# Kernel optimization log

Measured on AMD Instinct MI355X. Metric: run time of the kernel, lower is better.

Reference implementation:

```python
import jax, jax.numpy as jnp
import numpy as np

NUM_TAGS = 5

def setup_inputs() -> dict:
    key = jax.random.key(0)
    ks = jax.random.split(key, 8)
    B, N, K, Q = 2, 5, 5, 4
    Ls, Lq, D = 128, 128, 768
    inp = {
        'support_token_embedding': jax.random.normal(ks[0], (B * N * K, Ls, D), jnp.float32),
        'query_token_embedding': jax.random.normal(ks[1], (B * N * Q, Lq, D), jnp.float32),
        'support_mask': jnp.ones((B * N * K, Ls), jnp.float32),
        'query_mask': jnp.ones((B * N * Q, Lq), jnp.float32),
        'support_entity_label': jax.random.normal(ks[2], (B * N * K, Ls, NUM_TAGS), jnp.float32),
        'proj_w': jax.random.normal(ks[3], (D, 4 * D), jnp.float32) * 0.02,
        'proj_b': jnp.zeros((D,), jnp.float32),
        'rel_w1': jax.random.normal(ks[4], (D, 4 * D), jnp.float32) * 0.02,
        'rel_b1': jnp.zeros((D,), jnp.float32),
        'rel_w2': jax.random.normal(ks[5], (1, D), jnp.float32) * 0.02,
        'rel_b2': jnp.zeros((1,), jnp.float32),
        'B': B, 'N': N, 'K': K, 'Q': Q,
    }
    return inp

def _fuse(m1, m2):
    return jnp.concatenate([m1, m2, jnp.abs(m1 - m2), m1 * m2], axis=-1)

def reference(support_token_embedding, query_token_embedding, support_mask, query_mask,
              support_entity_label, proj_w, proj_b, rel_w1, rel_b1, rel_w2, rel_b2,
              B, N, K, Q):
    D = support_token_embedding.shape[-1]
    Lq = query_token_embedding.shape[1]

    # ---- cal_bio: per-(sample,shot) tag prototypes, vectorized ----
    labels = jnp.argmax(support_entity_label, axis=-1)                 # [BNK, Ls]
    onehot = jax.nn.one_hot(labels, NUM_TAGS, dtype=jnp.float32)       # [BNK, Ls, T]
    # tag 0 ('O') is additionally gated by the support mask
    masks = jnp.concatenate([onehot[:, :, :1] * support_mask[:, :, None], onehot[:, :, 1:]], axis=2)
    sums = jnp.einsum('blt,bld->btd', masks, support_token_embedding)  # [BNK, T, D]
    cnt = jnp.sum(masks, axis=1)[:, :, None]                           # [BNK, T, 1]
    proto = jnp.where(cnt > 0, sums / jnp.maximum(cnt, 1.0), 0.0)      # [BNK, T, D]
    proto = proto.reshape(B * N, K, NUM_TAGS, D).mean(axis=1)          # mean over K shots
    proto = proto.reshape(B, N, NUM_TAGS, D)                           # support_BIO

    # ---- expand to all (query, class) pairs: batch = B*N*Q*N ----
    BQ = B * N * Q * N
    support = jnp.broadcast_to(proto[:, None], (B, N * Q, N, NUM_TAGS, D)).reshape(BQ, NUM_TAGS, D)
    query = jnp.broadcast_to(query_token_embedding.reshape(B, N * Q, 1, Lq, D),
                             (B, N * Q, N, Lq, D)).reshape(BQ, Lq, D)
    qmask = jnp.broadcast_to(query_mask.reshape(B, N * Q, 1, Lq),
                             (B, N * Q, N, Lq)).reshape(BQ, Lq, 1)
    smask = jnp.ones((BQ, NUM_TAGS, 1), jnp.float32)

    # ---- CoAttention with additive mask bias + post-softmax mask multiply ----
    att = jnp.einsum('bsd,bqd->bsq', support, query) + smask * jnp.swapaxes(qmask, 1, 2) * 100.0
    support_ = jnp.einsum('bsq,bqd->bsd', jax.nn.softmax(att, axis=2), query) * smask
    query_ = jnp.einsum('bqs,bsd->bqd', jax.nn.softmax(jnp.swapaxes(att, 1, 2), axis=2), support) * qmask

    # ---- fuse + proj + relu ----
    es = jax.nn.relu(_fuse(support, support_) @ proj_w.T + proj_b)     # [BQ, T, D]
    eq = jax.nn.relu(_fuse(query, query_) @ proj_w.T + proj_b)        # [BQ, Lq, D]

    # ---- local aggregation: masked max + mean pooling ----
    eq_agg = jnp.concatenate([jnp.max(eq, axis=1), jnp.sum(eq, axis=1) / jnp.sum(qmask, axis=1)], axis=1)
    es_agg = jnp.concatenate([jnp.max(es, axis=1), jnp.sum(es, axis=1) / jnp.sum(smask, axis=1)], axis=1)

    # ---- relation MLP ----
    cat_seq = jnp.concatenate([eq_agg, es_agg], axis=1)                # [BQ, 4D]
    h = jax.nn.relu(cat_seq @ rel_w1.T + rel_b1)
    logits = h @ rel_w2.T + rel_b2                                     # [BQ, 1]
    return logits.reshape(B * N * Q, N)
```

## Files before the change

### kernel.cpp

```cpp
#include <hip/hip_runtime.h>

typedef unsigned short u16;
typedef __attribute__((ext_vector_type(8))) short short8;
typedef __attribute__((ext_vector_type(4))) float f32x4;

#define B_   2
#define N_   5
#define K_   5
#define Q_   4
#define T_   5
#define D_   768
#define L_   128
#define BN_  (B_*N_)
#define BNK_ (B_*N_*K_)
#define BQ_  (B_*N_*Q_*N_)
#define K4_  (4*D_)
#define KFQ  1536
#define AROWS 144

#define QEMB_N  (40*128*768)
#define PROJW_N (768*3072)
#define R_PROTO1 5120
#define R_SUP    5248
#define R_PROTO2 6248
#define R_TOTAL  6400

__device__ __forceinline__ float bf2f(u16 u) {
    return __uint_as_float(((unsigned)u) << 16);
}
__device__ __forceinline__ u16 f2bf(float f) {
    unsigned u = __float_as_uint(f);
    return (u16)((u + 0x7fffu + ((u >> 16) & 1u)) >> 16);
}
__device__ __forceinline__ void gl_lds16(const u16* g, u16* l) {
    __builtin_amdgcn_global_load_lds(
        (const __attribute__((address_space(1))) unsigned int*)g,
        (__attribute__((address_space(3))) unsigned int*)l, 16, 0, 0);
}

__global__ void k_convert3(const float* __restrict__ q, const float* __restrict__ pw,
                           const float* __restrict__ rw, u16* __restrict__ qo,
                           u16* __restrict__ po, u16* __restrict__ ro) {
    const long n1 = QEMB_N / 4, n2 = PROJW_N / 4;
    const long total = n1 + 2 * n2;
    for (long i = (long)blockIdx.x * 256 + threadIdx.x; i < total; i += (long)gridDim.x * 256) {
        const float* src; u16* dst; long k;
        if (i < n1)            { src = q;  dst = qo; k = i; }
        else if (i < n1 + n2)  { src = pw; dst = po; k = i - n1; }
        else                   { src = rw; dst = ro; k = i - n1 - n2; }
        float4 v = ((const float4*)src)[k];
        u16 o[4] = {f2bf(v.x), f2bf(v.y), f2bf(v.z), f2bf(v.w)};
        *(uint2*)(dst + k * 4) = *(const uint2*)o;
    }
}

__global__ void k_proto_shot(const float* __restrict__ label, const float* __restrict__ smask,
                             const float* __restrict__ semb, float* __restrict__ proto_shot) {
    int bnk = blockIdx.x;
    int s = blockIdx.y;
    __shared__ int   s_tag[L_];
    __shared__ float s_w[L_];
    __shared__ float s_cnt[T_];
    int tid = threadIdx.x;
    if (tid < L_) {
        const float* lp = label + ((long)bnk * L_ + tid) * T_;
        float best = lp[0]; int bi = 0;
        #pragma unroll
        for (int t = 1; t < T_; ++t) { float v = lp[t]; if (v > best) { best = v; bi = t; } }
        s_tag[tid] = bi;
        s_w[tid]   = (bi == 0) ? smask[(long)bnk * L_ + tid] : 1.0f;
    }
    __syncthreads();
    if (tid < T_) {
        float c = 0.f;
        for (int l = 0; l < L_; ++l) if (s_tag[l] == tid) c += s_w[l];
        s_cnt[tid] = c;
    }
    __syncthreads();
    float acc[T_] = {};
    for (int l = 0; l < L_; ++l) {
        float w = s_w[l]; int tg = s_tag[l];
        float e = semb[((long)bnk * L_ + l) * D_ + tid + s * 256] * w;
        #pragma unroll
        for (int t = 0; t < T_; ++t) acc[t] += (tg == t) ? e : 0.0f;
    }
    int d = tid + s * 256;
    #pragma unroll
    for (int t = 0; t < T_; ++t) {
        float c = s_cnt[t];
        float v = (c > 0.f) ? acc[t] / fmaxf(c, 1.f) : 0.f;
        proto_shot[(bnk * T_ + t) * D_ + d] = v;
    }
}

__global__ void k_proto_mean(const float* __restrict__ proto_shot,
                             float* __restrict__ proto_f32, u16* __restrict__ A_all) {
    int bx = blockIdx.x;
    if (bx < 150) {
        int idx = bx * 256 + threadIdx.x;
        if (idx >= BN_ * T_ * D_) return;
        int r = idx / D_, d = idx - r * D_;
        int bn = r / T_;
        int rem = idx - bn * (T_ * D_);
        float s = 0.f;
        #pragma unroll
        for (int k = 0; k < K_; ++k) s += proto_shot[(bn * K_ + k) * (T_ * D_) + rem];
        s *= (1.f / K_);
        proto_f32[idx] = s;
        u16 b = f2bf(s);
        A_all[(size_t)(R_PROTO1 + r) * D_ + d] = b;
        A_all[(size_t)(R_PROTO2 + r) * D_ + d] = b;
    } else {
        int zidx = (bx - 150) * 256 + threadIdx.x;
        if (zidx >= 59904 + 78336) return;
        size_t off;
        if (zidx < 59904) off = (size_t)5170 * D_ + zidx;
        else              off = (size_t)6298 * D_ + (zidx - 59904);
        A_all[off] = 0;
    }
}

__global__ void k_attn(const float* __restrict__ qemb, const float* __restrict__ qmask_g,
                       const float* __restrict__ proto_f32,
                       u16* __restrict__ qf, u16* __restrict__ supA,
                       float* __restrict__ p2m_ws, float* __restrict__ qssum_ws) {
    int x = blockIdx.x;
    int xcd = x & 7, slot = x >> 3;
    int g = (slot / 5) * 8 + xcd;
    int n2 = slot % 5;
    int bq = g * 5 + n2;
    int q_idx = g;
    int bn = (bq / (N_ * Q_ * N_)) * N_ + (bq % N_);
    __shared__ float s_proto[T_ * D_];
    __shared__ float s_att[T_][L_];
    __shared__ float s_ps[T_][L_];
    __shared__ float s_p2[L_][8];
    __shared__ float s_qm[L_];
    int tid = threadIdx.x;
    int w = tid >> 6, lane = tid & 63;
    for (int i = tid; i < T_ * D_; i += 256) s_proto[i] = proto_f32[bn * T_ * D_ + i];
    if (tid < L_) s_qm[tid] = qmask_g[(long)q_idx * L_ + tid];
    __syncthreads();
    for (int p = tid; p < T_ * L_; p += 256) {
        int t = p >> 7, q = p & (L_ - 1);
        const float* pp = s_proto + t * D_;
        const float4* qp = (const float4*)(qemb + ((size_t)q_idx * L_ + q) * D_);
        float acc = 0.f;
        #pragma unroll 4
        for (int d = 0; d < D_ / 4; ++d) {
            float4 v = qp[d];
            acc += v.x * pp[4 * d] + v.y * pp[4 * d + 1] + v.z * pp[4 * d + 2] + v.w * pp[4 * d + 3];
        }
        s_att[t][q] = acc + 100.f * s_qm[q];
    }
    __syncthreads();
    if (tid < T_) {
        int t = tid; float m = -1e30f;
        for (int q = 0; q < L_; ++q) m = fmaxf(m, s_att[t][q]);
        float ss = 0.f;
        for (int q = 0; q < L_; ++q) { float e = __expf(s_att[t][q] - m); s_ps[t][q] = e; ss += e; }
        float inv = 1.f / ss;
        for (int q = 0; q < L_; ++q) s_ps[t][q] *= inv;
    } else if (tid >= 128) {
        int q = tid - 128; float m = -1e30f;
        float e[T_];
        #pragma unroll
        for (int t = 0; t < T_; ++t) m = fmaxf(m, s_att[t][q]);
        float ss = 0.f;
        #pragma unroll
        for (int t = 0; t < T_; ++t) { e[t] = __expf(s_att[t][q] - m); ss += e[t]; }
        float inv = s_qm[q] / ss;
        #pragma unroll
        for (int t = 0; t < T_; ++t) {
            s_p2[q][t] = e[t] * inv;
            p2m_ws[((size_t)bq * T_ + t) * L_ + q] = e[t] * inv;
        }
    } else if (tid == 5) {
        float s = 0.f;
        for (int q = 0; q < L_; ++q) s += s_qm[q];
        qssum_ws[bq] = s;
    }
    __syncthreads();
    u16* qfb = qf + (size_t)bq * AROWS * KFQ;
    {
        float acc[T_][3] = {};
        #pragma unroll 4
        for (int q = 0; q < L_; ++q) {
            const float* qp = qemb + ((size_t)q_idx * L_ + q) * D_;
            float qv[3];
            #pragma unroll
            for (int s = 0; s < 3; ++s) qv[s] = qp[tid + s * 256];
            #pragma unroll
            for (int t = 0; t < T_; ++t) {
                float p = s_ps[t][q];
                #pragma unroll
                for (int s = 0; s < 3; ++s) acc[t][s] += p * qv[s];
            }
        }
        #pragma unroll
        for (int t = 0; t < T_; ++t) {
            u16* er = qfb + (size_t)(128 + t) * KFQ;
            #pragma unroll
            for (int s = 0; s < 3; ++s) {
                int d = tid + s * 256;
                float p = s_proto[t * D_ + d];
                float sv = acc[t][s];
                supA[((size_t)bq * T_ + t) * D_ + d] = f2bf(sv);
                er[d]       = f2bf(fabsf(p - sv));
                er[768 + d] = f2bf(p * sv);
            }
        }
    }
    for (int rr = 0; rr < 32; ++rr) {
        int row = w * 32 + rr;
        float p0 = s_p2[row][0], p1 = s_p2[row][1], p2v = s_p2[row][2];
        float p3 = s_p2[row][3], p4 = s_p2[row][4];
        const float* qrow = qemb + ((size_t)q_idx * L_ + row) * D_;
        u16* qr = qfb + (size_t)row * KFQ;
        #pragma unroll
        for (int ch = 0; ch < 12; ++ch) {
            int c = ch * 64 + lane;
            float m2 = p0 * s_proto[c] + p1 * s_proto[D_ + c] + p2v * s_proto[2 * D_ + c]
                     + p3 * s_proto[3 * D_ + c] + p4 * s_proto[4 * D_ + c];
            float qv = qrow[c];
            qr[c]       = f2bf(fabsf(qv - m2));
            qr[768 + c] = f2bf(qv * m2);
        }
    }
    {
        u16* pr2 = qfb + (size_t)133 * KFQ;
        short8 z = short8{0, 0, 0, 0, 0, 0, 0, 0};
        for (int i = tid; i < (11 * KFQ) / 8; i += 256) *(short8*)(pr2 + i * 8) = z;
    }
}

#define SUBGW ((128 + 128) * 32)
__global__ __launch_bounds__(256) void k_gemm_gw(const u16* __restrict__ A_all,
                                                 const u16* __restrict__ projw_bf,
                                                 u16* __restrict__ g1, u16* __restrict__ sw2,
                                                 u16* __restrict__ pw2) {
    int mbase = blockIdx.y * 128;
    int jbase = blockIdx.x * 128;
    int boff = (mbase >= R_SUP) ? 768 : 0;
    __shared__ __align__(16) u16 sT[2][2 * SUBGW];
    int tid = threadIdx.x;
    int lane = tid & 63, w = tid >> 6, quad = lane >> 4, l16 = lane & 15;
    int srow = lane >> 2, sko = lane & 3;
    const u16* Ab = A_all + ((size_t)mbase + srow) * D_ + sko * 8;
    const u16* Bb = projw_bf + (size_t)(jbase + srow) * K4_ + boff + sko * 8;

    f32x4 zero = {0.f, 0.f, 0.f, 0.f};
    f32x4 acc[8][2];
    #pragma unroll
    for (int rt = 0; rt < 8; ++rt) { acc[rt][0] = zero; acc[rt][1] = zero; }

    auto issue = [&](int kt, int b) {
        #pragma unroll
        for (int s = 0; s < 2; ++s) {
            int k0 = kt * 64 + s * 32;
            u16* base = sT[b] + s * SUBGW;
            gl_lds16(Ab + (size_t)(w * 16) * D_ + k0, base + (w * 16) * 32);
            gl_lds16(Ab + (size_t)(64 + w * 16) * D_ + k0, base + (64 + w * 16) * 32);
            gl_lds16(Bb + (size_t)(w * 16) * K4_ + k0, base + (128 + w * 16) * 32);
            gl_lds16(Bb + (size_t)(64 + w * 16) * K4_ + k0, base + (128 + 64 + w * 16) * 32);
        }
    };

    issue(0, 0);
    for (int kt = 0; kt < D_ / 64; ++kt) {
        int cur = kt & 1;
        __syncthreads();
        if (kt + 1 < D_ / 64) issue(kt + 1, 1 - cur);
        #pragma unroll
        for (int s = 0; s < 2; ++s) {
            const u16* base = sT[cur] + s * SUBGW;
            short8 bfr[2];
            #pragma unroll
            for (int jj = 0; jj < 2; ++jj)
                bfr[jj] = *(const short8*)(base + (128 + (w * 2 + jj) * 16 + l16) * 32 + quad * 8);
            #pragma unroll
            for (int rt = 0; rt < 8; ++rt) {
                short8 a = *(const short8*)(base + (rt * 16 + l16) * 32 + quad * 8);
                acc[rt][0] = __builtin_amdgcn_mfma_f32_16x16x32_bf16(a, bfr[0], acc[rt][0], 0, 0, 0);
                acc[rt][1] = __builtin_amdgcn_mfma_f32_16x16x32_bf16(a, bfr[1], acc[rt][1], 0, 0, 0);
            }
        }
    }
    #pragma unroll
    for (int jj = 0; jj < 2; ++jj) {
        int col = jbase + (w * 2 + jj) * 16 + l16;
        #pragma unroll
        for (int rt = 0; rt < 8; ++rt)
            #pragma unroll
            for (int r = 0; r < 4; ++r) {
                int row = mbase + rt * 16 + quad * 4 + r;
                u16 v = f2bf(acc[rt][jj][r]);
                if (row < R_SUP)            g1[(size_t)row * D_ + col] = v;
                else if (row < R_PROTO2)    sw2[(size_t)(row - R_SUP) * D_ + col] = v;
                else if (row < R_PROTO2+50) pw2[(size_t)(row - R_PROTO2) * D_ + col] = v;
            }
    }
}

#define SUBSZ ((AROWS + 128) * 32)
__global__ __launch_bounds__(256) void k_gemm_q(
        const u16* __restrict__ qf, const u16* __restrict__ projw_bf,
        const float* __restrict__ projb, const u16* __restrict__ g1,
        const u16* __restrict__ pw2, const u16* __restrict__ sw2,
        const float* __restrict__ p2m, const float* __restrict__ qssum_ws,
        u16* __restrict__ cat_ws) {
    int x = blockIdx.x;
    int xcd = x & 7, slot = x >> 3;
    int i = slot / 6, jslot = slot % 6;
    int g = (i / 5) * 8 + xcd;
    int bq = g * 5 + (i % 5);
    int jbase = jslot * 128;
    int q_idx = bq / N_;
    int bn = (bq / (N_ * Q_ * N_)) * N_ + (bq % N_);
    __shared__ __align__(16) u16 sT[2][2 * SUBSZ];
    __shared__ float s_p2mL[T_ * 128];
    __shared__ float s_pw2L[T_ * 128];
    int tid = threadIdx.x;
    int lane = tid & 63, w = tid >> 6, quad = lane >> 4, l16 = lane & 15;
    int srow = lane >> 2, sko = lane & 3;
    const u16* Ab = qf + ((size_t)bq * AROWS + srow) * KFQ + sko * 8;
    const u16* Bb = projw_bf + (size_t)(jbase + srow) * K4_ + 1536 + sko * 8;

    f32x4 zero = {0.f, 0.f, 0.f, 0.f};
    f32x4 acc[9][2];
    #pragma unroll
    for (int rt = 0; rt < 9; ++rt) { acc[rt][0] = zero; acc[rt][1] = zero; }

    auto issue = [&](int kt, int b) {
        #pragma unroll
        for (int s = 0; s < 2; ++s) {
            int k0 = kt * 64 + s * 32;
            u16* base = sT[b] + s * SUBSZ;
            gl_lds16(Ab + (size_t)(w * 16) * KFQ + k0, base + (w * 16) * 32);
            gl_lds16(Ab + (size_t)(64 + w * 16) * KFQ + k0, base + (64 + w * 16) * 32);
            if (w == 0) gl_lds16(Ab + (size_t)128 * KFQ + k0, base + 128 * 32);
            gl_lds16(Bb + (size_t)(w * 16) * K4_ + k0, base + (AROWS + w * 16) * 32);
            gl_lds16(Bb + (size_t)(64 + w * 16) * K4_ + k0, base + (AROWS + 64 + w * 16) * 32);
        }
    };

    issue(0, 0);
    for (int kt = 0; kt < KFQ / 64; ++kt) {
        int cur = kt & 1;
        __syncthreads();
        if (kt + 1 < KFQ / 64) issue(kt + 1, 1 - cur);
        #pragma unroll
        for (int s = 0; s < 2; ++s) {
            const u16* base = sT[cur] + s * SUBSZ;
            short8 bfr[2];
            #pragma unroll
            for (int jj = 0; jj < 2; ++jj)
                bfr[jj] = *(const short8*)(base + (AROWS + (w * 2 + jj) * 16 + l16) * 32 + quad * 8);
            #pragma unroll
            for (int rt = 0; rt < 9; ++rt) {
                short8 a = *(const short8*)(base + (rt * 16 + l16) * 32 + quad * 8);
                acc[rt][0] = __builtin_amdgcn_mfma_f32_16x16x32_bf16(a, bfr[0], acc[rt][0], 0, 0, 0);
                acc[rt][1] = __builtin_amdgcn_mfma_f32_16x16x32_bf16(a, bfr[1], acc[rt][1], 0, 0, 0);
            }
        }
    }
    for (int i2 = tid; i2 < T_ * 128; i2 += 256) {
        s_p2mL[i2] = p2m[(size_t)bq * (T_ * 128) + i2];
        s_pw2L[i2] = bf2f(pw2[(size_t)(bn * T_ + (i2 >> 7)) * D_ + jbase + (i2 & 127)]);
    }
    __syncthreads();
    float inv_qs = 1.f / qssum_ws[bq];
    #pragma unroll
    for (int jj = 0; jj < 2; ++jj) {
        int col = jbase + (w * 2 + jj) * 16 + l16;
        int cj = (w * 2 + jj) * 16 + l16;
        float bias = projb[col];
        float qmax = 0.f, qsum = 0.f, smax = 0.f, ssum = 0.f;
        #pragma unroll
        for (int rt = 0; rt < 8; ++rt) {
            #pragma unroll
            for (int r = 0; r < 4; ++r) {
                int row = rt * 16 + quad * 4 + r;
                float g1v = bf2f(g1[(size_t)(q_idx * 128 + row) * D_ + col]);
                float mix = s_p2mL[row] * s_pw2L[cj]
                          + s_p2mL[128 + row] * s_pw2L[128 + cj]
                          + s_p2mL[256 + row] * s_pw2L[256 + cj]
                          + s_p2mL[384 + row] * s_pw2L[384 + cj]
                          + s_p2mL[512 + row] * s_pw2L[512 + cj];
                float v = fmaxf(acc[rt][jj][r] + g1v + mix + bias, 0.f);
                qmax = fmaxf(qmax, v); qsum += v;
            }
        }
        #pragma unroll
        for (int r = 0; r < 4; ++r) {
            int t = quad * 4 + r;
            if (t < T_) {
                float g1v = bf2f(g1[(size_t)(5120 + bn * T_ + t) * D_ + col]);
                float s2v = bf2f(sw2[(size_t)(bq * T_ + t) * D_ + col]);
                float v = fmaxf(acc[8][jj][r] + g1v + s2v + bias, 0.f);
                smax = fmaxf(smax, v); ssum += v;
            }
        }
        qmax = fmaxf(qmax, __shfl_xor(qmax, 16, 64)); qmax = fmaxf(qmax, __shfl_xor(qmax, 32, 64));
        qsum += __shfl_xor(qsum, 16, 64);             qsum += __shfl_xor(qsum, 32, 64);
        smax = fmaxf(smax, __shfl_xor(smax, 16, 64)); smax = fmaxf(smax, __shfl_xor(smax, 32, 64));
        ssum += __shfl_xor(ssum, 16, 64);             ssum += __shfl_xor(ssum, 32, 64);
        if (quad == 0) {
            u16* cp = cat_ws + (size_t)bq * K4_;
            cp[col]           = f2bf(qmax);
            cp[D_ + col]      = f2bf(qsum * inv_qs);
            cp[2 * D_ + col]  = f2bf(smax);
            cp[3 * D_ + col]  = f2bf(ssum * 0.2f);
        }
    }
}

#define AST  40
__global__ __launch_bounds__(256) void k_relmlp(const u16* __restrict__ cat_ws,
                                                const u16* __restrict__ w1,
                                                float* __restrict__ part) {
    int mbase = blockIdx.y * 64;
    int jbase = blockIdx.x * 128;
    int ks = blockIdx.z;
    __shared__ __align__(16) u16 sA[64 * AST];
    __shared__ __align__(16) u16 sB[128 * AST];
    int tid = threadIdx.x;
    int lane = tid & 63, w = tid >> 6, quad = lane >> 4, l16 = lane & 15;
    f32x4 zero = {0.f, 0.f, 0.f, 0.f};
    f32x4 acc[4][2];
    #pragma unroll
    for (int rt = 0; rt < 4; ++rt) { acc[rt][0] = zero; acc[rt][1] = zero; }

    for (int kt = ks * 12; kt < ks * 12 + 12; ++kt) {
        int k0 = kt * 32;
        __syncthreads();
        {
            int row = tid >> 2, ko = (tid & 3) * 8;
            int grow = mbase + row;
            short8 val = short8{0, 0, 0, 0, 0, 0, 0, 0};
            if (grow < BQ_) val = *(const short8*)(cat_ws + (size_t)grow * K4_ + k0 + ko);
            *(short8*)(sA + row * AST + ko) = val;
        }
        for (int u = tid; u < 512; u += 256) {
            int row = u >> 2, ko = (u & 3) * 8;
            *(short8*)(sB + row * AST + ko) =
                *(const short8*)(w1 + (size_t)(jbase + row) * K4_ + k0 + ko);
        }
        __syncthreads();
        short8 af[4], bfr[2];
        #pragma unroll
        for (int rt = 0; rt < 4; ++rt)
            af[rt] = *(const short8*)(sA + (rt * 16 + l16) * AST + quad * 8);
        #pragma unroll
        for (int jj = 0; jj < 2; ++jj)
            bfr[jj] = *(const short8*)(sB + ((2 * w + jj) * 16 + l16) * AST + quad * 8);
        #pragma unroll
        for (int rt = 0; rt < 4; ++rt)
            #pragma unroll
            for (int jj = 0; jj < 2; ++jj)
                acc[rt][jj] = __builtin_amdgcn_mfma_f32_16x16x32_bf16(af[rt], bfr[jj], acc[rt][jj], 0, 0, 0);
    }
    #pragma unroll
    for (int jj = 0; jj < 2; ++jj) {
        int col = jbase + (2 * w + jj) * 16 + l16;
        #pragma unroll
        for (int rt = 0; rt < 4; ++rt) {
            #pragma unroll
            for (int r = 0; r < 4; ++r) {
                int grow = mbase + rt * 16 + quad * 4 + r;
                if (grow < BQ_)
                    part[((size_t)ks * BQ_ + grow) * D_ + col] = acc[rt][jj][r];
            }
        }
    }
}

__global__ void k_rel_fin(const float* __restrict__ part, const float* __restrict__ b1,
                          const float* __restrict__ w2, const float* __restrict__ b2,
                          float* __restrict__ out) {
    int bq = blockIdx.x, tid = threadIdx.x;
    float a = 0.f;
    #pragma unroll
    for (int s = 0; s < 3; ++s) {
        int col = tid + s * 256;
        float sum = 0.f;
        #pragma unroll
        for (int ks = 0; ks < 8; ++ks) sum += part[((size_t)ks * BQ_ + bq) * D_ + col];
        float h = fmaxf(sum + b1[col], 0.f);
        a += h * w2[col];
    }
    __shared__ float red[256];
    red[tid] = a; __syncthreads();
    for (int off = 128; off >= 1; off >>= 1) {
        if (tid < off) red[tid] += red[tid + off];
        __syncthreads();
    }
    if (tid == 0) out[bq] = red[0] + b2[0];
}

extern "C" void kernel_launch(void* const* d_in, const int* in_sizes, int n_in,
                              void* d_out, int out_size, void* d_ws, size_t ws_size,
                              hipStream_t stream) {
    (void)in_sizes; (void)n_in; (void)out_size; (void)ws_size;
    const float* semb  = (const float*)d_in[0];
    const float* qemb  = (const float*)d_in[1];
    const float* smask = (const float*)d_in[2];
    const float* qmask = (const float*)d_in[3];
    const float* label = (const float*)d_in[4];
    const float* projw = (const float*)d_in[5];
    const float* projb = (const float*)d_in[6];
    const float* relw1 = (const float*)d_in[7];
    const float* relb1 = (const float*)d_in[8];
    const float* relw2 = (const float*)d_in[9];
    const float* relb2 = (const float*)d_in[10];

    char* ws = (char*)d_ws;
    u16*   A_all     = (u16*)  (ws + 0);
    u16*   projw_bf  = (u16*)  (ws + 9830400);
    u16*   relw1_bf  = (u16*)  (ws + 14548992);
    float* proto_shot= (float*)(ws + 19267584);
    float* proto_f32 = (float*)(ws + 20035584);
    float* qssum     = (float*)(ws + 20189184);
    float* p2m_ws    = (float*)(ws + 20190080);
    u16*   pw2_ws    = (u16*)  (ws + 20702080);
    u16*   sw2_ws    = (u16*)  (ws + 20778880);
    u16*   cat_ws    = (u16*)  (ws + 22314880);
    u16*   g1_ws     = (u16*)  (ws + 23543680);
    float* part_ws   = (float*)(ws + 31604608);
    u16*   qf_ws     = (u16*)  (ws + 36519808);

    k_convert3<<<2048, 256, 0, stream>>>(qemb, projw, relw1, A_all, projw_bf, relw1_bf);
    k_proto_shot<<<dim3(BNK_, 3), 256, 0, stream>>>(label, smask, semb, proto_shot);
    k_proto_mean<<<691, 256, 0, stream>>>(proto_shot, proto_f32, A_all);
    k_attn<<<BQ_, 256, 0, stream>>>(qemb, qmask, proto_f32, qf_ws, A_all + (size_t)R_SUP * D_,
                                    p2m_ws, qssum);
    k_gemm_gw<<<dim3(6, 50), 256, 0, stream>>>(A_all, projw_bf, g1_ws, sw2_ws, pw2_ws);
    k_gemm_q<<<1200, 256, 0, stream>>>(qf_ws, projw_bf, projb, g1_ws, pw2_ws, sw2_ws,
                                       p2m_ws, qssum, cat_ws);
    k_relmlp<<<dim3(6, 4, 8), 256, 0, stream>>>(cat_ws, relw1_bf, part_ws);
    k_rel_fin<<<BQ_, 256, 0, stream>>>(part_ws, relb1, relw2, relb2, (float*)d_out);
}
```

Measured before the change: 463.4 us.

## Load GEMM fragments directly from global into registers, dropping LDS staging

The query-projection GEMM kernel no longer stages A and B tiles through double-buffered shared memory with block barriers. Each wave now loads its MFMA operand fragments straight from global memory into registers, with a two-stage register ping-pong to overlap loads and MFMAs. This removes the LDS traffic and __syncthreads. In exchange, all four waves redundantly load the same 144 A rows from global/L2, uses more VGPRs, and issues narrower strided global loads.

```diff
diff --git a/kernel.cpp b/kernel.cpp
--- a/kernel.cpp
+++ b/kernel.cpp
@@ -302,7 +302,6 @@
     }
 }
 
-#define SUBSZ ((AROWS + 128) * 32)
 __global__ __launch_bounds__(256) void k_gemm_q(
         const u16* __restrict__ qf, const u16* __restrict__ projw_bf,
         const float* __restrict__ projb, const u16* __restrict__ g1,
@@ -317,52 +316,43 @@
     int jbase = jslot * 128;
     int q_idx = bq / N_;
     int bn = (bq / (N_ * Q_ * N_)) * N_ + (bq % N_);
-    __shared__ __align__(16) u16 sT[2][2 * SUBSZ];
     __shared__ float s_p2mL[T_ * 128];
     __shared__ float s_pw2L[T_ * 128];
     int tid = threadIdx.x;
     int lane = tid & 63, w = tid >> 6, quad = lane >> 4, l16 = lane & 15;
-    int srow = lane >> 2, sko = lane & 3;
-    const u16* Ab = qf + ((size_t)bq * AROWS + srow) * KFQ + sko * 8;
-    const u16* Bb = projw_bf + (size_t)(jbase + srow) * K4_ + 1536 + sko * 8;
+
+    const u16* Abase = qf + ((size_t)bq * AROWS + l16) * KFQ + quad * 8;
+    const u16* Bbase = projw_bf + (size_t)(jbase + w * 32 + l16) * K4_ + 1536 + quad * 8;
 
     f32x4 zero = {0.f, 0.f, 0.f, 0.f};
     f32x4 acc[9][2];
     #pragma unroll
     for (int rt = 0; rt < 9; ++rt) { acc[rt][0] = zero; acc[rt][1] = zero; }
 
-    auto issue = [&](int kt, int b) {
-        #pragma unroll
-        for (int s = 0; s < 2; ++s) {
-            int k0 = kt * 64 + s * 32;
-            u16* base = sT[b] + s * SUBSZ;
-            gl_lds16(Ab + (size_t)(w * 16) * KFQ + k0, base + (w * 16) * 32);
-            gl_lds16(Ab + (size_t)(64 + w * 16) * KFQ + k0, base + (64 + w * 16) * 32);
-            if (w == 0) gl_lds16(Ab + (size_t)128 * KFQ + k0, base + 128 * 32);
-            gl_lds16(Bb + (size_t)(w * 16) * K4_ + k0, base + (AROWS + w * 16) * 32);
-            gl_lds16(Bb + (size_t)(64 + w * 16) * K4_ + k0, base + (AROWS + 64 + w * 16) * 32);
-        }
+    short8 a0[9], b0[2], a1[9], b1[2];
+    auto loadf = [&](short8* A, short8* Bf, int kt) {
+        int k0 = kt * 32;
+        #pragma unroll
+        for (int rt = 0; rt < 9; ++rt)
+            A[rt] = *(const short8*)(Abase + (size_t)rt * 16 * KFQ + k0);
+        #pragma unroll
+        for (int jj = 0; jj < 2; ++jj)
+            Bf[jj] = *(const short8*)(Bbase + (size_t)jj * 16 * K4_ + k0);
     };
-
-    issue(0, 0);
-    for (int kt = 0; kt < KFQ / 64; ++kt) {
-        int cur = kt & 1;
-        __syncthreads();
-        if (kt + 1 < KFQ / 64) issue(kt + 1, 1 - cur);
-        #pragma unroll
-        for (int s = 0; s < 2; ++s) {
-            const u16* base = sT[cur] + s * SUBSZ;
-            short8 bfr[2];
-            #pragma unroll
-            for (int jj = 0; jj < 2; ++jj)
-                bfr[jj] = *(const short8*)(base + (AROWS + (w * 2 + jj) * 16 + l16) * 32 + quad * 8);
-            #pragma unroll
-            for (int rt = 0; rt < 9; ++rt) {
-                short8 a = *(const short8*)(base + (rt * 16 + l16) * 32 + quad * 8);
-                acc[rt][0] = __builtin_amdgcn_mfma_f32_16x16x32_bf16(a, bfr[0], acc[rt][0], 0, 0, 0);
-                acc[rt][1] = __builtin_amdgcn_mfma_f32_16x16x32_bf16(a, bfr[1], acc[rt][1], 0, 0, 0);
-            }
-        }
+    auto domfma = [&](short8* A, short8* Bf) {
+        #pragma unroll
+        for (int rt = 0; rt < 9; ++rt) {
+            acc[rt][0] = __builtin_amdgcn_mfma_f32_16x16x32_bf16(A[rt], Bf[0], acc[rt][0], 0, 0, 0);
+            acc[rt][1] = __builtin_amdgcn_mfma_f32_16x16x32_bf16(A[rt], Bf[1], acc[rt][1], 0, 0, 0);
+        }
+    };
+
+    loadf(a0, b0, 0);
+    for (int kt = 0; kt < KFQ / 32; kt += 2) {
+        loadf(a1, b1, kt + 1);
+        domfma(a0, b0);
+        if (kt + 2 < KFQ / 32) loadf(a0, b0, kt + 2);
+        domfma(a1, b1);
     }
     for (int i2 = tid; i2 < T_ * 128; i2 += 256) {
         s_p2mL[i2] = p2m[(size_t)bq * (T_ * 128) + i2];
```

Result: slower. 606.3 us (+30.8%).

## Split query-feature build out of k_attn and pipeline relmlp loads via direct LDS

Applied to the files above, without the earlier changes.

The per-row query fusion (|q-m2|, q*m2) moves from the 200-block attention kernel into a new k_qf kernel launched on a 200x4 grid, so the largest bf16 write phase runs with four times as many blocks. k_qf reads the softmax weights back from the p2m workspace instead of shared memory and reloads the prototypes. The relation MLP GEMM now uses double-buffered global-to-LDS direct loads with 64-wide k steps instead of synchronous register-staged tiles. In exchange there is an extra launch, redundant prototype loads, and the relmlp tile loads no longer zero-pad rows beyond BQ.

```diff
diff --git a/kernel.cpp b/kernel.cpp
--- a/kernel.cpp
+++ b/kernel.cpp
@@ -134,10 +134,8 @@
     __shared__ float s_proto[T_ * D_];
     __shared__ float s_att[T_][L_];
     __shared__ float s_ps[T_][L_];
-    __shared__ float s_p2[L_][8];
     __shared__ float s_qm[L_];
     int tid = threadIdx.x;
-    int w = tid >> 6, lane = tid & 63;
     for (int i = tid; i < T_ * D_; i += 256) s_proto[i] = proto_f32[bn * T_ * D_ + i];
     if (tid < L_) s_qm[tid] = qmask_g[(long)q_idx * L_ + tid];
     __syncthreads();
@@ -171,10 +169,7 @@
         for (int t = 0; t < T_; ++t) { e[t] = __expf(s_att[t][q] - m); ss += e[t]; }
         float inv = s_qm[q] / ss;
         #pragma unroll
-        for (int t = 0; t < T_; ++t) {
-            s_p2[q][t] = e[t] * inv;
-            p2m_ws[((size_t)bq * T_ + t) * L_ + q] = e[t] * inv;
-        }
+        for (int t = 0; t < T_; ++t) p2m_ws[((size_t)bq * T_ + t) * L_ + q] = e[t] * inv;
     } else if (tid == 5) {
         float s = 0.f;
         for (int q = 0; q < L_; ++q) s += s_qm[q];
@@ -211,10 +206,36 @@
             }
         }
     }
-    for (int rr = 0; rr < 32; ++rr) {
-        int row = w * 32 + rr;
-        float p0 = s_p2[row][0], p1 = s_p2[row][1], p2v = s_p2[row][2];
-        float p3 = s_p2[row][3], p4 = s_p2[row][4];
+    {
+        u16* pr2 = qfb + (size_t)133 * KFQ;
+        short8 z = short8{0, 0, 0, 0, 0, 0, 0, 0};
+        for (int i = tid; i < (11 * KFQ) / 8; i += 256) *(short8*)(pr2 + i * 8) = z;
+    }
+}
+
+__global__ void k_qf(const float* __restrict__ qemb, const float* __restrict__ proto_f32,
+                     const float* __restrict__ p2m, u16* __restrict__ qf) {
+    int bq = blockIdx.x;
+    int rg = blockIdx.y;
+    int q_idx = bq / N_;
+    int bn = (bq / (N_ * Q_ * N_)) * N_ + (bq % N_);
+    __shared__ float s_proto[T_ * D_];
+    __shared__ float s_p2[32][8];
+    int tid = threadIdx.x;
+    int w = tid >> 6, lane = tid & 63;
+    for (int i = tid; i < T_ * D_; i += 256) s_proto[i] = proto_f32[bn * T_ * D_ + i];
+    if (tid < 32 * T_) {
+        int r = tid / T_, t = tid - r * T_;
+        s_p2[r][t] = p2m[((size_t)bq * T_ + t) * L_ + rg * 32 + r];
+    }
+    __syncthreads();
+    u16* qfb = qf + (size_t)bq * AROWS * KFQ;
+    #pragma unroll
+    for (int rr = 0; rr < 8; ++rr) {
+        int rloc = w * 8 + rr;
+        int row = rg * 32 + rloc;
+        float p0 = s_p2[rloc][0], p1 = s_p2[rloc][1], p2v = s_p2[rloc][2];
+        float p3 = s_p2[rloc][3], p4 = s_p2[rloc][4];
         const float* qrow = qemb + ((size_t)q_idx * L_ + row) * D_;
         u16* qr = qfb + (size_t)row * KFQ;
         #pragma unroll
@@ -226,11 +247,6 @@
             qr[c]       = f2bf(fabsf(qv - m2));
             qr[768 + c] = f2bf(qv * m2);
         }
-    }
-    {
-        u16* pr2 = qfb + (size_t)133 * KFQ;
-        short8 z = short8{0, 0, 0, 0, 0, 0, 0, 0};
-        for (int i = tid; i < (11 * KFQ) / 8; i += 256) *(short8*)(pr2 + i * 8) = z;
     }
 }
 
@@ -415,50 +431,55 @@
     }
 }
 
-#define AST  40
+#define SUBRM ((64 + 128) * 32)
 __global__ __launch_bounds__(256) void k_relmlp(const u16* __restrict__ cat_ws,
                                                 const u16* __restrict__ w1,
                                                 float* __restrict__ part) {
     int mbase = blockIdx.y * 64;
     int jbase = blockIdx.x * 128;
     int ks = blockIdx.z;
-    __shared__ __align__(16) u16 sA[64 * AST];
-    __shared__ __align__(16) u16 sB[128 * AST];
+    __shared__ __align__(16) u16 sT[2][2 * SUBRM];
     int tid = threadIdx.x;
     int lane = tid & 63, w = tid >> 6, quad = lane >> 4, l16 = lane & 15;
+    int srow = lane >> 2, sko = lane & 3;
+    const u16* Ab = cat_ws + (size_t)(mbase + srow) * K4_ + ks * 384 + sko * 8;
+    const u16* Bb = w1 + (size_t)(jbase + srow) * K4_ + ks * 384 + sko * 8;
+
     f32x4 zero = {0.f, 0.f, 0.f, 0.f};
     f32x4 acc[4][2];
     #pragma unroll
     for (int rt = 0; rt < 4; ++rt) { acc[rt][0] = zero; acc[rt][1] = zero; }
 
-    for (int kt = ks * 12; kt < ks * 12 + 12; ++kt) {
-        int k0 = kt * 32;
+    auto issue = [&](int kt, int b) {
+        #pragma unroll
+        for (int s = 0; s < 2; ++s) {
+            int k0 = kt * 64 + s * 32;
+            u16* base = sT[b] + s * SUBRM;
+            gl_lds16(Ab + (size_t)(w * 16) * K4_ + k0, base + (w * 16) * 32);
+            gl_lds16(Bb + (size_t)(w * 16) * K4_ + k0, base + (64 + w * 16) * 32);
+            gl_lds16(Bb + (size_t)(64 + w * 16) * K4_ + k0, base + (64 + 64 + w * 16) * 32);
+        }
+    };
+
+    issue(0, 0);
+    for (int kt = 0; kt < 6; ++kt) {
+        int cur = kt & 1;
         __syncthreads();
-        {
-            int row = tid >> 2, ko = (tid & 3) * 8;
-            int grow = mbase + row;
-            short8 val = short8{0, 0, 0, 0, 0, 0, 0, 0};
-            if (grow < BQ_) val = *(const short8*)(cat_ws + (size_t)grow * K4_ + k0 + ko);
-            *(short8*)(sA + row * AST + ko) = val;
-        }
-        for (int u = tid; u < 512; u += 256) {
-            int row = u >> 2, ko = (u & 3) * 8;
-            *(short8*)(sB + row * AST + ko) =
-                *(const short8*)(w1 + (size_t)(jbase + row) * K4_ + k0 + ko);
-        }
-        __syncthreads();
-        short8 af[4], bfr[2];
-        #pragma unroll
-        for (int rt = 0; rt < 4; ++rt)
-            af[rt] = *(const short8*)(sA + (rt * 16 + l16) * AST + quad * 8);
-        #pragma unroll
-        for (int jj = 0; jj < 2; ++jj)
-            bfr[jj] = *(const short8*)(sB + ((2 * w + jj) * 16 + l16) * AST + quad * 8);
-        #pragma unroll
-        for (int rt = 0; rt < 4; ++rt)
+        if (kt + 1 < 6) issue(kt + 1, 1 - cur);
+        #pragma unroll
+        for (int s = 0; s < 2; ++s) {
+            const u16* base = sT[cur] + s * SUBRM;
+            short8 bfr[2];
             #pragma unroll
             for (int jj = 0; jj < 2; ++jj)
-                acc[rt][jj] = __builtin_amdgcn_mfma_f32_16x16x32_bf16(af[rt], bfr[jj], acc[rt][jj], 0, 0, 0);
+                bfr[jj] = *(const short8*)(base + (64 + (2 * w + jj) * 16 + l16) * 32 + quad * 8);
+            #pragma unroll
+            for (int rt = 0; rt < 4; ++rt) {
+                short8 a = *(const short8*)(base + (rt * 16 + l16) * 32 + quad * 8);
+                acc[rt][0] = __builtin_amdgcn_mfma_f32_16x16x32_bf16(a, bfr[0], acc[rt][0], 0, 0, 0);
+                acc[rt][1] = __builtin_amdgcn_mfma_f32_16x16x32_bf16(a, bfr[1], acc[rt][1], 0, 0, 0);
+            }
+        }
     }
     #pragma unroll
     for (int jj = 0; jj < 2; ++jj) {
@@ -534,6 +555,7 @@
     k_proto_mean<<<691, 256, 0, stream>>>(proto_shot, proto_f32, A_all);
     k_attn<<<BQ_, 256, 0, stream>>>(qemb, qmask, proto_f32, qf_ws, A_all + (size_t)R_SUP * D_,
                                     p2m_ws, qssum);
+    k_qf<<<dim3(BQ_, 4), 256, 0, stream>>>(qemb, proto_f32, p2m_ws, qf_ws);
     k_gemm_gw<<<dim3(6, 50), 256, 0, stream>>>(A_all, projw_bf, g1_ws, sw2_ws, pw2_ws);
     k_gemm_q<<<1200, 256, 0, stream>>>(qf_ws, projw_bf, projb, g1_ws, pw2_ws, sw2_ws,
                                        p2m_ws, qssum, cat_ws);
```

Measured after the change: 483.5 us. 1.04x slower.
